# Performance work log

Measured on AMD Instinct MI355X. Metric: run time of the kernel, lower is better.

## Reference

```python
import jax, jax.numpy as jnp
import numpy as np

B, L, D, C, N, K = 4096, 4096, 1024, 64, 8192, 5
TEMP = 0.1
ALPHA = 2.0
EPS = 1e-12


def setup_inputs() -> dict:
    key = jax.random.key(0)
    ks = jax.random.split(key, 8)
    x = jax.random.normal(ks[0], (B, 1, L), jnp.float32)
    y = jax.random.randint(ks[1], (B,), 0, C)
    Wf = jax.random.normal(ks[2], (L, D), jnp.float32) * 0.02
    Wc = jax.random.normal(ks[3], (C, D), jnp.float32) * 0.02
    bc = jnp.zeros((C,), jnp.float32)
    supports_old = jax.random.normal(ks[4], (N, D), jnp.float32)
    scores_old = jax.nn.softmax(jax.random.normal(ks[5], (N, C), jnp.float32), axis=-1)
    labels_old = jax.nn.one_hot(jax.random.randint(ks[6], (N,), 0, C), C, dtype=jnp.float32)
    return dict(x=x, y=y, Wf=Wf, Wc=Wc, bc=bc, supports_old=supports_old,
                labels_old=labels_old, scores_old=scores_old)


def _l2n(v, axis):
    return v / jnp.maximum(jnp.linalg.norm(v, axis=axis, keepdims=True), EPS)


def _masked_mean(v, w):
    return jnp.sum(v * w) / jnp.maximum(jnp.sum(w), 1.0)


def _tta_loss(x, Wf, Wc, bc, supports_old, labels_old, scores_old):
    feats = x.reshape(B, L) @ Wf                      # [B, D] featurizer
    logits = feats @ Wc.T + bc                        # [B, C]
    probs = jax.nn.softmax(logits, -1)
    logp = jax.nn.log_softmax(logits, -1)
    prob = probs.max(-1)
    pred = jnp.argmax(logits, -1)
    # prediction-confidence filter
    y_certain = prob >= prob.mean()
    # input-energy entropy filter (scipy.stats.entropy over axis=2)
    px = x * x
    px = px / jnp.maximum(px.sum(2, keepdims=True), EPS)
    e = -(px * jnp.log(px + 1e-30)).sum(2).reshape(B)
    e_certain = e < e.mean()
    w_c = (e_certain & y_certain).astype(jnp.float32)  # certain mask as weights
    w_u = 1.0 - w_c
    yhat = jax.nn.one_hot(pred, C, dtype=jnp.float32)
    # --- memory bank concat + prototype build (no_grad in torch) ---
    sup_all = jnp.concatenate([supports_old, feats], 0)        # [N+B, D]
    lab_all = jnp.concatenate([labels_old, yhat], 0)           # [N+B, C]
    w_all = jnp.concatenate([jnp.ones((N,), jnp.float32), w_c], 0)
    lw = lab_all * w_all[:, None]
    protos = _l2n(sup_all, 1).T @ lw / jnp.maximum(lw.sum(0, keepdims=True), EPS)
    protos = jax.lax.stop_gradient(_l2n(protos, 0))            # [D, C]
    # --- loss1: Tsallis entropy - diversity on balanced probs ---
    m = jnp.sum(probs * w_c[:, None], 0) / jnp.maximum(w_c.sum(), 1.0)
    pb = probs / jnp.maximum(m, EPS)
    pb = pb / pb.sum(1, keepdims=True)
    tsallis = jnp.mean((1.0 - jnp.sum(pb ** ALPHA, 1)) / (ALPHA - 1.0))
    pm = pb.mean(0)
    div = -jnp.sum(pm * jnp.log(pm + EPS))
    loss1 = tsallis - div
    # --- loss2: PCL, prototype CE on certain samples (temp=1) ---
    lp = jax.nn.log_softmax(_l2n(feats, 1) @ protos, -1)       # [B, C]
    ce = -jnp.take_along_axis(lp, pred[:, None], 1)[:, 0]
    loss2 = _masked_mean(ce, w_c)
    # --- loss3: NCL, kNN soft targets from memory bank, uncertain rows ---
    scores_all = jax.lax.stop_gradient(jnp.concatenate([scores_old, probs], 0))
    sup_det = jax.lax.stop_gradient(sup_all)
    sim = _l2n(feats, 1) @ _l2n(sup_det, 1).T / TEMP           # [B, N+B]
    sim = jnp.where(w_all[None, :] > 0, sim, -jnp.inf)
    _, idx = jax.lax.top_k(sim, K)                             # [B, K]
    tgt = scores_all[idx].mean(1)                              # [B, C]
    ncl = -(tgt * logp).sum(1)
    loss3 = _masked_mean(ncl, w_u)
    return loss1 + loss2 + loss3


def reference(x, y, Wf, Wc, bc, supports_old, labels_old, scores_old):
    return _tta_loss(x, Wf, Wc, bc, supports_old, labels_old, scores_old)
```

## Files before the change

### kernel.cpp

```cpp
#include <hip/hip_runtime.h>
#include <math.h>

#define BBATCH 4096
#define LLEN   4096
#define DDIM   1024
#define CCLS   64
#define NSUP   8192
#define NTOT   12288
#define FEPS   1e-12f
#define KCHUNK 48
#define KCAND  (KCHUNK*5)

#define SC_SUMP  0
#define SC_SUME  1
#define SC_SUMWC 2
#define SC_TSAL  3
#define SC_L2NUM 4
#define SC_L3NUM 5

typedef _Float16 half4_t __attribute__((ext_vector_type(4)));
typedef _Float16 half8_t __attribute__((ext_vector_type(8)));
typedef float    f32x4   __attribute__((ext_vector_type(4)));
typedef float    f32x16  __attribute__((ext_vector_type(16)));

static const size_t OFF_FEATS  = 0;
static const size_t OFF_FEATP1 = OFF_FEATS  + (size_t)BBATCH*DDIM;
static const size_t OFF_WFTH   = OFF_FEATP1 + (size_t)BBATCH*DDIM;
static const size_t OFF_WFTL   = OFF_WFTH   + (size_t)DDIM*LLEN/2;
static const size_t OFF_PROBS  = OFF_WFTL   + (size_t)DDIM*LLEN/2;
static const size_t OFF_LOGP   = OFF_PROBS  + (size_t)BBATCH*CCLS;
static const size_t OFF_FNORM  = OFF_LOGP   + (size_t)BBATCH*CCLS;
static const size_t OFF_SNORM  = OFF_FNORM  + BBATCH;
static const size_t OFF_PMAX   = OFF_SNORM  + NSUP;
static const size_t OFF_EROW   = OFF_PMAX   + BBATCH;
static const size_t OFF_WC     = OFF_EROW   + BBATCH;
static const size_t OFF_PRED   = OFF_WC     + BBATCH;
static const size_t OFF_RB     = OFF_PRED   + BBATCH;
static const size_t OFF_SNM    = OFF_RB     + BBATCH;
static const size_t OFF_PROTOT = OFF_SNM    + NTOT;
static const size_t OFF_CVAL   = OFF_PROTOT + (size_t)CCLS*DDIM;
static const size_t OFF_CIDX   = OFF_CVAL   + (size_t)BBATCH*KCAND;
static const size_t OFF_ZERO   = OFF_CIDX   + (size_t)BBATCH*KCAND;
static const size_t OFF_MACC   = OFF_ZERO;
static const size_t OFF_PMACC  = OFF_MACC   + CCLS;
static const size_t OFF_COLS   = OFF_PMACC  + CCLS;
static const size_t OFF_SCAL   = OFF_COLS   + CCLS;
static const size_t OFF_PROTUN = OFF_SCAL   + 32;
static const size_t OFF_ZEND   = OFF_PROTUN + (size_t)DDIM*CCLS;
static const size_t OFF_SUPH   = OFF_ZEND;
static const size_t OFF_SUPL   = OFF_SUPH   + (size_t)NSUP*DDIM/2;
static const size_t WS_END     = OFF_SUPL   + (size_t)NSUP*DDIM/2;

__device__ __forceinline__ float waveSum(float v){
  #pragma unroll
  for (int o = 32; o > 0; o >>= 1) v += __shfl_xor(v, o);
  return v;
}
__device__ __forceinline__ float waveMax(float v){
  #pragma unroll
  for (int o = 32; o > 0; o >>= 1) v = fmaxf(v, __shfl_xor(v, o));
  return v;
}
__device__ __forceinline__ float blockSum256(float v, float* sh4){
  v = waveSum(v);
  if ((threadIdx.x & 63) == 0) sh4[threadIdx.x >> 6] = v;
  __syncthreads();
  float r = sh4[0] + sh4[1] + sh4[2] + sh4[3];
  __syncthreads();
  return r;
}
__device__ __forceinline__ void top5_insert(float* v, int* ix, float s, int si){
  bool c0 = s > v[0], c1 = s > v[1], c2 = s > v[2], c3 = s > v[3], c4 = s > v[4];
  v[4] = c4 ? (c3 ? v[3] : s) : v[4];  ix[4] = c4 ? (c3 ? ix[3] : si) : ix[4];
  v[3] = c3 ? (c2 ? v[2] : s) : v[3];  ix[3] = c3 ? (c2 ? ix[2] : si) : ix[3];
  v[2] = c2 ? (c1 ? v[1] : s) : v[2];  ix[2] = c2 ? (c1 ? ix[1] : si) : ix[2];
  v[1] = c1 ? (c0 ? v[0] : s) : v[1];  ix[1] = c1 ? (c0 ? ix[0] : si) : ix[1];
  v[0] = c0 ? s : v[0];                ix[0] = c0 ? si : ix[0];
}
__device__ __forceinline__ void split4(const float4 v, half4_t* h, half4_t* l){
  half4_t hh, ll;
  hh[0] = (_Float16)v.x; hh[1] = (_Float16)v.y; hh[2] = (_Float16)v.z; hh[3] = (_Float16)v.w;
  ll[0] = (_Float16)(v.x - (float)hh[0]);
  ll[1] = (_Float16)(v.y - (float)hh[1]);
  ll[2] = (_Float16)(v.z - (float)hh[2]);
  ll[3] = (_Float16)(v.w - (float)hh[3]);
  *h = hh; *l = ll;
}
__device__ __forceinline__ void split8(const float4 a, const float4 b,
                                       half8_t* h, half8_t* l){
  half8_t hh, ll;
  hh[0]=(_Float16)a.x; hh[1]=(_Float16)a.y; hh[2]=(_Float16)a.z; hh[3]=(_Float16)a.w;
  hh[4]=(_Float16)b.x; hh[5]=(_Float16)b.y; hh[6]=(_Float16)b.z; hh[7]=(_Float16)b.w;
  ll[0]=(_Float16)(a.x-(float)hh[0]); ll[1]=(_Float16)(a.y-(float)hh[1]);
  ll[2]=(_Float16)(a.z-(float)hh[2]); ll[3]=(_Float16)(a.w-(float)hh[3]);
  ll[4]=(_Float16)(b.x-(float)hh[4]); ll[5]=(_Float16)(b.y-(float)hh[5]);
  ll[6]=(_Float16)(b.z-(float)hh[6]); ll[7]=(_Float16)(b.w-(float)hh[7]);
  *h = hh; *l = ll;
}

__global__ __launch_bounds__(256)
void k_entropy(const float* __restrict__ x, float* __restrict__ e_row,
               float* __restrict__ scal){
  __shared__ __align__(16) float lx[LLEN];
  __shared__ float sh4[4];
  int row = blockIdx.x, t = threadIdx.x;
  const float4* xr = (const float4*)(x + (size_t)row * LLEN);
  float s = 0.f;
  #pragma unroll
  for (int i = 0; i < 4; ++i){
    float4 v = xr[t + 256*i];
    ((float4*)lx)[t + 256*i] = v;
    s += v.x*v.x + v.y*v.y + v.z*v.z + v.w*v.w;
  }
  s = blockSum256(s, sh4);
  float inv = 1.0f / fmaxf(s, FEPS);
  float ent = 0.f;
  #pragma unroll
  for (int i = 0; i < 4; ++i){
    float4 v = ((float4*)lx)[t + 256*i];
    float p;
    p = v.x*v.x*inv; ent -= p * logf(p + 1e-30f);
    p = v.y*v.y*inv; ent -= p * logf(p + 1e-30f);
    p = v.z*v.z*inv; ent -= p * logf(p + 1e-30f);
    p = v.w*v.w*inv; ent -= p * logf(p + 1e-30f);
  }
  ent = blockSum256(ent, sh4);
  if (t == 0){ e_row[row] = ent; atomicAdd(&scal[SC_SUME], ent); }
}

__global__ __launch_bounds__(256)
void k_wft(const float* __restrict__ Wf, unsigned short* __restrict__ WftH,
           unsigned short* __restrict__ WftL){
  __shared__ __align__(16) float ld[64*68];
  int t = threadIdx.x;
  int d0 = blockIdx.x * 64;
  int l0 = blockIdx.y * 64;
  #pragma unroll
  for (int i = 0; i < 4; ++i){
    int flat = t + 256*i;
    int l = flat >> 4, d4 = (flat & 15) * 4;
    *(float4*)&ld[l*68 + d4] = *(const float4*)(Wf + (size_t)(l0+l)*DDIM + d0 + d4);
  }
  __syncthreads();
  #pragma unroll
  for (int i = 0; i < 4; ++i){
    int flat = t + 256*i;
    int d = flat >> 4, l4 = (flat & 15) * 4;
    float4 v = make_float4(ld[(l4+0)*68 + d], ld[(l4+1)*68 + d],
                           ld[(l4+2)*68 + d], ld[(l4+3)*68 + d]);
    half4_t h, l;
    split4(v, &h, &l);
    *(half4_t*)(WftH + (size_t)(d0+d)*LLEN + l0 + l4) = h;
    *(half4_t*)(WftL + (size_t)(d0+d)*LLEN + l0 + l4) = l;
  }
}

#define SUBH 4096

__global__ __launch_bounds__(256)
void k_feats_mfma(const float* __restrict__ X, const unsigned short* __restrict__ WftHu,
                  const unsigned short* __restrict__ WftLu, float* __restrict__ featp){
  __shared__ __align__(16) _Float16 lds[2*4*SUBH];
  int t = threadIdx.x;
  int n0 = blockIdx.x * 128;
  int m0 = blockIdx.y * 128;
  int kz = blockIdx.z;
  int w = t >> 6, lane = t & 63;
  int wr = w >> 1, wc = w & 1;
  int l31 = lane & 31, hi = lane >> 5;
  const _Float16* Bgh = (const _Float16*)WftHu + (size_t)n0*LLEN;
  const _Float16* Bgl = (const _Float16*)WftLu + (size_t)n0*LLEN;
  const size_t glRow = (size_t)(lane >> 2)*LLEN;
  int ra = t >> 1;
  int kg8 = (t & 1) * 16;
  int aswz = (ra >> 3) & 3;
  const float* Ag = X + (size_t)(m0 + ra)*LLEN + kg8;
  f32x16 acc[2][2];
  #pragma unroll
  for (int i=0;i<2;++i){
    #pragma unroll
    for (int j=0;j<2;++j) acc[i][j] = (f32x16)(0.f);
  }
  const int kstart = kz*2048;

  #define STAGE_B(bufi, k0c) do {                                                 \
    _Float16* Lb = lds + (bufi)*(4*SUBH);                                         \
    _Pragma("unroll")                                                             \
    for (int s2 = 0; s2 < 2; ++s2){                                               \
      int blk = s2*4 + w;                                                         \
      int csrc = (lane & 3) ^ ((blk*2 + (lane >> 5)) & 3);                        \
      size_t go = glRow + (size_t)blk*16*LLEN + (k0c) + (size_t)csrc*8;           \
      __builtin_amdgcn_global_load_lds(                                           \
        (const __attribute__((address_space(1))) void*)(Bgh + go),                \
        (__attribute__((address_space(3))) void*)(Lb + 2*SUBH + blk*512), 16,0,0);\
      __builtin_amdgcn_global_load_lds(                                           \
        (const __attribute__((address_space(1))) void*)(Bgl + go),                \
        (__attribute__((address_space(3))) void*)(Lb + 3*SUBH + blk*512), 16,0,0);\
    }                                                                             \
  } while(0)

  STAGE_B(0, kstart);
  float4 avs[4];
  #pragma unroll
  for (int i=0;i<4;++i) avs[i] = *(const float4*)(Ag + kstart + 4*i);
  int cur = 0;
  int swz = (l31 >> 3) & 3;
  for (int it = 0; it < 64; ++it){
    _Float16* Ah = lds + cur*(4*SUBH);
    _Float16* Al = Ah + SUBH;
    #pragma unroll
    for (int c2 = 0; c2 < 2; ++c2){
      half8_t hv, lv;
      split8(avs[2*c2], avs[2*c2+1], &hv, &lv);
      int slot = ((kg8 >> 3) + c2) ^ aswz;
      *(half8_t*)&Ah[ra*32 + slot*8] = hv;
      *(half8_t*)&Al[ra*32 + slot*8] = lv;
    }
    __syncthreads();
    if (it < 63){
      int kn = kstart + (it+1)*32;
      STAGE_B(cur ^ 1, kn);
      #pragma unroll
      for (int i=0;i<4;++i) avs[i] = *(const float4*)(Ag + kn + 4*i);
      __builtin_amdgcn_sched_barrier(0);
    }
    const _Float16* Bh = lds + cur*(4*SUBH) + 2*SUBH;
    const _Float16* Bl = Bh + SUBH;
    #pragma unroll
    for (int kf = 0; kf < 2; ++kf){
      int sc = (kf*2 + hi) ^ swz;
      half8_t ahf[2], alf[2], bhf[2], blf[2];
      #pragma unroll
      for (int mi=0;mi<2;++mi){
        int off = (wr*64 + mi*32 + l31)*32 + sc*8;
        ahf[mi] = *(const half8_t*)&Ah[off];
        alf[mi] = *(const half8_t*)&Al[off];
      }
      #pragma unroll
      for (int ni=0;ni<2;++ni){
        int off = (wc*64 + ni*32 + l31)*32 + sc*8;
        bhf[ni] = *(const half8_t*)&Bh[off];
        blf[ni] = *(const half8_t*)&Bl[off];
      }
      #pragma unroll
      for (int mi=0;mi<2;++mi){
        #pragma unroll
        for (int ni=0;ni<2;++ni){
          acc[mi][ni] = __builtin_amdgcn_mfma_f32_32x32x16_f16(ahf[mi], bhf[ni], acc[mi][ni], 0,0,0);
          acc[mi][ni] = __builtin_amdgcn_mfma_f32_32x32x16_f16(ahf[mi], blf[ni], acc[mi][ni], 0,0,0);
          acc[mi][ni] = __builtin_amdgcn_mfma_f32_32x32x16_f16(alf[mi], bhf[ni], acc[mi][ni], 0,0,0);
        }
      }
    }
    cur ^= 1;
  }
  #undef STAGE_B
  float* outp = featp + (size_t)kz * BBATCH * DDIM;
  #pragma unroll
  for (int mi=0;mi<2;++mi){
    #pragma unroll
    for (int ni=0;ni<2;++ni){
      #pragma unroll
      for (int r=0;r<16;++r){
        int row = m0 + wr*64 + mi*32 + (r&3) + 8*(r>>2) + 4*hi;
        int col = n0 + wc*64 + ni*32 + l31;
        outp[(size_t)row*DDIM + col] = acc[mi][ni][r];
      }
    }
  }
}

__global__ __launch_bounds__(256)
void k_supnorm(const float* __restrict__ sup, float* __restrict__ snorm,
               _Float16* __restrict__ suph, _Float16* __restrict__ supl){
  int w = threadIdx.x >> 6, lane = threadIdx.x & 63;
  int row = blockIdx.x*4 + w;
  const float4* rp = (const float4*)(sup + (size_t)row * DDIM);
  float s = 0.f;
  #pragma unroll
  for (int j=0;j<4;++j){
    float4 v = rp[lane + 64*j];
    half4_t h, l;
    split4(v, &h, &l);
    *(half4_t*)(suph + (size_t)row*DDIM + (lane + 64*j)*4) = h;
    *(half4_t*)(supl + (size_t)row*DDIM + (lane + 64*j)*4) = l;
    s += v.x*v.x+v.y*v.y+v.z*v.z+v.w*v.w;
  }
  s = waveSum(s);
  if (lane==0) snorm[row] = sqrtf(s);
}

__global__ __launch_bounds__(256)
void k_logits(float* __restrict__ feats, const float* __restrict__ featp1,
              const float* __restrict__ Wc,
              const float* __restrict__ bc, float* __restrict__ probs,
              float* __restrict__ logp, float* __restrict__ pmax,
              int* __restrict__ pred, float* __restrict__ fnorm,
              float* __restrict__ scal,
              _Float16* __restrict__ fh, _Float16* __restrict__ fl){
  __shared__ __align__(16) float f[DDIM];
  __shared__ float z[CCLS];
  __shared__ float sh4[4];
  int row = blockIdx.x, t = threadIdx.x;
  const float4* fr0 = (const float4*)(feats  + (size_t)row * DDIM);
  const float4* fr1 = (const float4*)(featp1 + (size_t)row * DDIM);
  float ss = 0.f;
  { float4 a = fr0[t], b = fr1[t];
    float4 v = make_float4(a.x+b.x, a.y+b.y, a.z+b.z, a.w+b.w);
    ((float4*)f)[t] = v;
    ((float4*)(feats + (size_t)row*DDIM))[t] = v;
    half4_t h, l;
    split4(v, &h, &l);
    *(half4_t*)(fh + (size_t)row*DDIM + t*4) = h;
    *(half4_t*)(fl + (size_t)row*DDIM + t*4) = l;
    ss += v.x*v.x+v.y*v.y+v.z*v.z+v.w*v.w; }
  ss = blockSum256(ss, sh4);
  if (t==0) fnorm[row] = sqrtf(ss);
  int w = t >> 6, lane = t & 63;
  for (int ci = 0; ci < 16; ++ci){
    int c = w*16 + ci;
    const float4* wc = (const float4*)(Wc + (size_t)c * DDIM);
    float d = 0.f;
    #pragma unroll
    for (int j=0;j<4;++j){
      float4 a = wc[lane + 64*j];
      float4 b = ((float4*)f)[lane + 64*j];
      d += a.x*b.x+a.y*b.y+a.z*b.z+a.w*b.w;
    }
    d = waveSum(d);
    if (lane == 0) z[c] = d + bc[c];
  }
  __syncthreads();
  if (w == 0){
    float zz = z[lane];
    float m = waveMax(zz);
    unsigned long long bal = __ballot(zz == m);
    int am = __ffsll(bal) - 1;
    float ex = expf(zz - m);
    float sv = waveSum(ex);
    probs[(size_t)row*CCLS + lane] = ex / sv;
    logp[(size_t)row*CCLS + lane]  = (zz - m) - logf(sv);
    if (lane == 0){
      float pmv = 1.0f / sv;
      pmax[row] = pmv;
      pred[row] = am;
      atomicAdd(&scal[SC_SUMP], pmv);
    }
  }
}

__global__ __launch_bounds__(256)
void k_mask(const float* __restrict__ e_row, const float* __restrict__ pmax,
            const float* __restrict__ fnorm, const float* __restrict__ snorm,
            const int* __restrict__ pred, float* __restrict__ w_c,
            float* __restrict__ rb, float* __restrict__ snm,
            float* __restrict__ colsum, float* __restrict__ scal){
  int i = blockIdx.x * 256 + threadIdx.x;
  if (i < NSUP) snm[i] = 1.0f / fmaxf(snorm[i], FEPS);
  if (i < BBATCH){
    float me = scal[SC_SUME] * (1.0f/BBATCH);
    float mp = scal[SC_SUMP] * (1.0f/BBATCH);
    float wc = ((e_row[i] < me) && (pmax[i] >= mp)) ? 1.0f : 0.0f;
    w_c[i] = wc;
    float fn = fmaxf(fnorm[i], FEPS);
    rb[i] = 10.0f / fn;
    snm[NSUP + i] = (wc > 0.f) ? (1.0f / fn) : -1.0f;
    atomicAdd(&scal[SC_SUMWC], wc);
    atomicAdd(&colsum[pred[i]], wc);
  }
}

__global__ __launch_bounds__(256)
void k_colsum_labels(const float* __restrict__ labels, float* __restrict__ colsum){
  int t = threadIdx.x, c = t & 63, sub = t >> 6;
  int r0 = blockIdx.x * 256;
  float s = 0.f;
  for (int i = 0; i < 64; ++i){
    int r = r0 + sub + 4*i;
    s += labels[(size_t)r*CCLS + c];
  }
  __shared__ float loc[4][64];
  loc[sub][c] = s;
  __syncthreads();
  if (sub == 0) atomicAdd(&colsum[c], loc[0][c]+loc[1][c]+loc[2][c]+loc[3][c]);
}

__global__ __launch_bounds__(256)
void k_m_accum(const float* __restrict__ probs, const float* __restrict__ w_c,
               float* __restrict__ m_acc){
  int t = threadIdx.x, c = t & 63, sub = t >> 6;
  int r0 = blockIdx.x * 64;
  float s = 0.f;
  for (int i = 0; i < 16; ++i){
    int r = r0 + sub + 4*i;
    s += probs[(size_t)r*CCLS + c] * w_c[r];
  }
  __shared__ float loc[4][64];
  loc[sub][c] = s;
  __syncthreads();
  if (sub == 0) atomicAdd(&m_acc[c], loc[0][c]+loc[1][c]+loc[2][c]+loc[3][c]);
}

__global__ __launch_bounds__(256)
void k_loss1(const float* __restrict__ probs, const float* __restrict__ m_acc,
             float* __restrict__ pm_acc, float* __restrict__ scal){
  int t = threadIdx.x, w = t >> 6, lane = t & 63;
  float swc = fmaxf(scal[SC_SUMWC], 1.0f);
  float minv = 1.0f / fmaxf(m_acc[lane] / swc, FEPS);
  float pml = 0.f, tsl = 0.f;
  int r0 = blockIdx.x * 64 + w * 16;
  for (int i = 0; i < 16; ++i){
    int r = r0 + i;
    float pb = probs[(size_t)r*CCLS + lane] * minv;
    float t1 = waveSum(pb);
    float t2 = waveSum(pb*pb);
    tsl += 1.0f - t2/(t1*t1);
    pml += pb/t1;
  }
  atomicAdd(&pm_acc[lane], pml);
  if (lane == 0) atomicAdd(&scal[SC_TSAL], tsl);
}

__global__ __launch_bounds__(256)
void k_protos_gemm(const float* __restrict__ sup, const float* __restrict__ feats,
                   const float* __restrict__ labels, const int* __restrict__ pred,
                   const float* __restrict__ w_c, const float* __restrict__ snm,
                   float* __restrict__ protos_un){
  __shared__ __align__(16) float ssx[64*68];
  __shared__ __align__(16) float sl[64*68];
  int t = threadIdx.x;
  int d0 = blockIdx.x * 64;
  int nbase = blockIdx.y * 1536;
  int dg = t & 15, cg = t >> 4;
  float acc[4][4];
  #pragma unroll
  for (int i=0;i<4;++i){
    #pragma unroll
    for (int j=0;j<4;++j) acc[i][j]=0.f;
  }
  for (int n0 = 0; n0 < 1536; n0 += 64){
    __syncthreads();
    #pragma unroll
    for (int i = 0; i < 4; ++i){
      int fidx = t + 256*i;
      int r = fidx >> 4;
      int dc = (fidx & 15) * 4;
      int n = nbase + n0 + r;
      const float* rp = (n < NSUP) ? (sup + (size_t)n*DDIM)
                                   : (feats + (size_t)(n-NSUP)*DDIM);
      *(float4*)&ssx[r*68 + dc] = *(const float4*)(rp + d0 + dc);
    }
    #pragma unroll
    for (int i = 0; i < 4; ++i){
      int fidx = t + 256*i;
      int r = fidx >> 4;
      int cc = (fidx & 15) * 4;
      int n = nbase + n0 + r;
      float sc = snm[n];
      float4 v;
      if (n < NSUP){
        float4 lb = *(const float4*)(labels + (size_t)n*CCLS + cc);
        v.x = lb.x*sc; v.y = lb.y*sc; v.z = lb.z*sc; v.w = lb.w*sc;
      } else {
        int b = n - NSUP;
        float base = w_c[b] * sc;
        int p = pred[b];
        v.x = (p == cc+0) ? base : 0.f;
        v.y = (p == cc+1) ? base : 0.f;
        v.z = (p == cc+2) ? base : 0.f;
        v.w = (p == cc+3) ? base : 0.f;
      }
      *(float4*)&sl[r*68 + cc] = v;
    }
    __syncthreads();
    #pragma unroll 4
    for (int kk = 0; kk < 64; ++kk){
      float4 a = *(float4*)&ssx[kk*68 + 4*dg];
      float4 b = *(float4*)&sl[kk*68 + 4*cg];
      float av[4] = {a.x,a.y,a.z,a.w};
      float bv[4] = {b.x,b.y,b.z,b.w};
      #pragma unroll
      for (int i=0;i<4;++i){
        #pragma unroll
        for (int j=0;j<4;++j) acc[i][j] = fmaf(av[i], bv[j], acc[i][j]);
      }
    }
  }
  #pragma unroll
  for (int i=0;i<4;++i){
    #pragma unroll
    for (int j=0;j<4;++j)
      atomicAdd(&protos_un[(size_t)(d0 + 4*dg + i)*CCLS + 4*cg + j], acc[i][j]);
  }
}

__global__ __launch_bounds__(256)
void k_protos_norm(const float* __restrict__ protos_un, const float* __restrict__ colsum,
                   float* __restrict__ protos_t){
  int c = blockIdx.x, t = threadIdx.x;
  __shared__ float sh4[4];
  float cs = fmaxf(colsum[c], FEPS);
  float v[4];
  float ss = 0.f;
  #pragma unroll
  for (int i=0;i<4;++i){
    int d = t + 256*i;
    v[i] = protos_un[(size_t)d*CCLS + c] / cs;
    ss += v[i]*v[i];
  }
  ss = blockSum256(ss, sh4);
  float inv = 1.0f / fmaxf(sqrtf(ss), FEPS);
  #pragma unroll
  for (int i=0;i<4;++i){
    int d = t + 256*i;
    protos_t[(size_t)c*DDIM + d] = v[i]*inv;
  }
}

__global__ __launch_bounds__(256)
void k_loss2(const float* __restrict__ feats, const float* __restrict__ protos_t,
             const int* __restrict__ pred, const float* __restrict__ w_c,
             const float* __restrict__ fnorm, float* __restrict__ scal){
  int row = blockIdx.x, t = threadIdx.x;
  float wc = w_c[row];
  if (wc == 0.f) return;
  __shared__ __align__(16) float f[DDIM];
  __shared__ float z[CCLS];
  float inv = 1.0f / fmaxf(fnorm[row], FEPS);
  { float4 v = ((const float4*)(feats + (size_t)row*DDIM))[t];
    v.x*=inv; v.y*=inv; v.z*=inv; v.w*=inv;
    ((float4*)f)[t] = v; }
  __syncthreads();
  int w = t >> 6, lane = t & 63;
  for (int ci=0; ci<16; ++ci){
    int c = w*16+ci;
    const float4* pc = (const float4*)(protos_t + (size_t)c*DDIM);
    float d = 0.f;
    #pragma unroll
    for (int j=0;j<4;++j){
      float4 a = pc[lane + 64*j];
      float4 b = ((float4*)f)[lane + 64*j];
      d += a.x*b.x+a.y*b.y+a.z*b.z+a.w*b.w;
    }
    d = waveSum(d);
    if (lane==0) z[c] = d;
  }
  __syncthreads();
  if (w == 0){
    float zz = z[lane];
    float m = waveMax(zz);
    float sv = waveSum(expf(zz - m));
    if (lane == 0){
      float lse = m + logf(sv);
      float ce = lse - z[pred[row]];
      atomicAdd(&scal[SC_L2NUM], ce * wc);
    }
  }
}

#define SIMTILES 32
__global__ __launch_bounds__(512, 2)
void k_sim_mfma(const _Float16* __restrict__ fh, const _Float16* __restrict__ fl,
                const _Float16* __restrict__ suph, const _Float16* __restrict__ supl,
                const float* __restrict__ rb, const float* __restrict__ snm,
                float* __restrict__ cval, int* __restrict__ cidx){
  __shared__ __align__(16) _Float16 lds[2*32768];
  __shared__ float sns[256];
  int t = threadIdx.x;
  int w = t >> 6, lane = t & 63;
  int wr = w >> 2, wcn = w & 3;
  int l31 = lane & 31, hi = lane >> 5;
  int bidl = blockIdx.y * 48 + blockIdx.x;
  int xcd = bidl & 7, lin = bidl >> 3;
  int yb = xcd * 2 + (lin / 48);
  int xb = lin - (lin / 48) * 48;
  int m0 = xb * 256, n0 = yb * 256;
  if (t < 256) sns[t] = snm[m0 + t];
  const _Float16 *Agh, *Agl;
  if (xb < 32){ Agh = suph + (size_t)m0*DDIM; Agl = supl + (size_t)m0*DDIM; }
  else        { Agh = fh + (size_t)(m0-NSUP)*DDIM; Agl = fl + (size_t)(m0-NSUP)*DDIM; }
  const _Float16* Bgh = fh + (size_t)n0*DDIM;
  const _Float16* Bgl = fl + (size_t)n0*DDIM;
  int Rlo = w*16 + (lane>>2), Rhi = 128 + Rlo;
  size_t offLo = (size_t)Rlo*DDIM + (size_t)((((lane&3) ^ ((Rlo>>3)&3))) * 8);
  size_t offHi = (size_t)Rhi*DDIM + (size_t)((((lane&3) ^ ((Rhi>>3)&3))) * 8);
  const _Float16* srcArr[4] = {Agh, Agl, Bgh, Bgl};
  f32x16 acc[4][2];
  #pragma unroll
  for (int i=0;i<4;++i){
    #pragma unroll
    for (int j=0;j<2;++j) acc[i][j] = (f32x16)(0.f);
  }

  #define SIM_STAGE(b, c, kt) do {                                                \
    const _Float16* sp = srcArr[(c)>>1] + (((c)&1) ? offHi : offLo)               \
                         + (size_t)(kt)*32;                                       \
    __builtin_amdgcn_global_load_lds(                                             \
      (const __attribute__((address_space(1))) void*)sp,                          \
      (__attribute__((address_space(3))) void*)(lds + (b)*32768 + ((c)>>1)*8192   \
                                                + ((c)&1)*4096 + w*512), 16,0,0); \
  } while(0)

  SIM_STAGE(0,0,0); SIM_STAGE(0,1,0); SIM_STAGE(0,2,0); SIM_STAGE(0,3,0);
  SIM_STAGE(0,4,0); SIM_STAGE(0,5,0); SIM_STAGE(0,6,0); SIM_STAGE(0,7,0);

  for (int kt = 0; kt < SIMTILES; ++kt){
    const _Float16* buf = lds + (kt&1)*32768;
    int nb = (kt+1)&1;
    asm volatile("s_waitcnt vmcnt(0)" ::: "memory");
    __builtin_amdgcn_s_barrier();
    __builtin_amdgcn_sched_barrier(0);
    half8_t bh[2][2], bl[2][2];
    #pragma unroll
    for (int ni=0;ni<2;++ni){
      int Rb = wcn*64 + ni*32 + l31;
      int swB = (Rb>>3)&3;
      const _Float16* pbh = buf + 16384 + Rb*32;
      const _Float16* pbl = buf + 24576 + Rb*32;
      #pragma unroll
      for (int k=0;k<2;++k){
        int s = ((k*2+hi)^swB)*8;
        bh[ni][k] = *(const half8_t*)(pbh + s);
        bl[ni][k] = *(const half8_t*)(pbl + s);
      }
    }
    #pragma unroll
    for (int p=0;p<4;++p){
      int Ra = wr*128 + p*32 + l31;
      int swA = (Ra>>3)&3;
      const _Float16* pah = buf + Ra*32;
      const _Float16* pal = buf + 8192 + Ra*32;
      half8_t ah[2], al[2];
      #pragma unroll
      for (int k=0;k<2;++k){
        int s = ((k*2+hi)^swA)*8;
        ah[k] = *(const half8_t*)(pah + s);
        al[k] = *(const half8_t*)(pal + s);
      }
      if (kt < SIMTILES-1){
        if (p==0){ SIM_STAGE(nb,0,kt+1); SIM_STAGE(nb,1,kt+1); }
        else if (p==1){ SIM_STAGE(nb,2,kt+1); SIM_STAGE(nb,3,kt+1); SIM_STAGE(nb,4,kt+1); }
        else if (p==2){ SIM_STAGE(nb,5,kt+1); SIM_STAGE(nb,6,kt+1); SIM_STAGE(nb,7,kt+1); }
      }
      __builtin_amdgcn_s_setprio(1);
      #pragma unroll
      for (int k=0;k<2;++k){
        #pragma unroll
        for (int ni=0;ni<2;++ni){
          acc[p][ni] = __builtin_amdgcn_mfma_f32_32x32x16_f16(ah[k], bh[ni][k], acc[p][ni], 0,0,0);
          acc[p][ni] = __builtin_amdgcn_mfma_f32_32x32x16_f16(ah[k], bl[ni][k], acc[p][ni], 0,0,0);
          acc[p][ni] = __builtin_amdgcn_mfma_f32_32x32x16_f16(al[k], bh[ni][k], acc[p][ni], 0,0,0);
        }
      }
      __builtin_amdgcn_s_setprio(0);
      __builtin_amdgcn_sched_barrier(0);
    }
  }
  #undef SIM_STAGE
  __syncthreads();
  float tv[2][5]; int ti[2][5];
  #pragma unroll
  for (int ni=0;ni<2;++ni){
    #pragma unroll
    for (int k=0;k<5;++k){ tv[ni][k] = -INFINITY; ti[ni][k] = 0x7fffffff; }
  }
  #pragma unroll
  for (int ni=0;ni<2;++ni){
    float rbv = rb[n0 + wcn*64 + ni*32 + l31];
    #pragma unroll
    for (int mi=0;mi<4;++mi){
      #pragma unroll
      for (int r=0;r<16;++r){
        int rl = wr*128 + mi*32 + (r&3) + 8*(r>>2) + 4*hi;
        float sn = sns[rl];
        float v = acc[mi][ni][r] * rbv * fabsf(sn);
        v = (sn > 0.f) ? v : -INFINITY;
        top5_insert(tv[ni], ti[ni], v, m0 + rl);
      }
    }
  }
  #pragma unroll
  for (int ni=0;ni<2;++ni){
    float pv[5]; int pi[5];
    #pragma unroll
    for (int k=0;k<5;++k){ pv[k] = __shfl_xor(tv[ni][k], 32); pi[k] = __shfl_xor(ti[ni][k], 32); }
    #pragma unroll
    for (int k=0;k<5;++k) top5_insert(tv[ni], ti[ni], pv[k], pi[k]);
  }
  float* MV = (float*)lds;
  int*   MI = (int*)(lds + 5120);
  if (hi == 0){
    #pragma unroll
    for (int ni=0;ni<2;++ni){
      int col = wcn*64 + ni*32 + l31;
      #pragma unroll
      for (int k=0;k<5;++k){
        MV[(col*2 + wr)*5 + k] = tv[ni][k];
        MI[(col*2 + wr)*5 + k] = ti[ni][k];
      }
    }
  }
  __syncthreads();
  if (t < 256){
    float bv[5]; int bi[5];
    #pragma unroll
    for (int k=0;k<5;++k){ bv[k] = MV[(t*2+0)*5 + k]; bi[k] = MI[(t*2+0)*5 + k]; }
    #pragma unroll
    for (int k=0;k<5;++k) top5_insert(bv, bi, MV[(t*2+1)*5 + k], MI[(t*2+1)*5 + k]);
    float* co = cval + (size_t)(n0 + t)*KCAND + xb*5;
    int*   ci = cidx + (size_t)(n0 + t)*KCAND + xb*5;
    #pragma unroll
    for (int k=0;k<5;++k){ co[k] = bv[k]; ci[k] = bi[k]; }
  }
}

__global__ __launch_bounds__(256)
void k_merge_ncl(const float* __restrict__ cval, const int* __restrict__ cidx,
                 const float* __restrict__ scores_old, const float* __restrict__ probs,
                 const float* __restrict__ logp, const float* __restrict__ w_c,
                 float* __restrict__ scal){
  int t = threadIdx.x, w = t >> 6, lane = t & 63;
  int b = blockIdx.x*4 + w;
  float bv[5]; int bi[5];
  #pragma unroll
  for (int k=0;k<5;++k){ bv[k] = -INFINITY; bi[k] = 0x7fffffff; }
  #pragma unroll
  for (int it = 0; it < 4; ++it){
    int j = lane + 64*it;
    if (j < KCAND)
      top5_insert(bv, bi, cval[(size_t)b*KCAND + j], cidx[(size_t)b*KCAND + j]);
  }
  #pragma unroll
  for (int off = 32; off > 0; off >>= 1){
    float pv[5]; int pi[5];
    #pragma unroll
    for (int k=0;k<5;++k){ pv[k] = __shfl_xor(bv[k], off); pi[k] = __shfl_xor(bi[k], off); }
    #pragma unroll
    for (int k=0;k<5;++k) top5_insert(bv, bi, pv[k], pi[k]);
  }
  float tg = 0.f;
  #pragma unroll
  for (int k=0;k<5;++k){
    int ix = bi[k];
    const float* srow = (ix < NSUP) ? (scores_old + (size_t)ix*CCLS)
                                    : (probs + (size_t)(ix-NSUP)*CCLS);
    tg += srow[lane];
  }
  tg *= 0.2f;
  float d = tg * logp[(size_t)b*CCLS + lane];
  d = waveSum(d);
  if (lane == 0) atomicAdd(&scal[SC_L3NUM], -d * (1.0f - w_c[b]));
}

__global__ void k_final(const float* __restrict__ pm_acc, const float* __restrict__ scal,
                        float* __restrict__ out){
  int lane = threadIdx.x;
  float pm = pm_acc[lane] * (1.0f/BBATCH);
  float dterm = pm * logf(pm + FEPS);
  float dv = waveSum(dterm);
  if (lane == 0){
    float div = -dv;
    float tsallis = scal[SC_TSAL] * (1.0f/BBATCH);
    float swc = scal[SC_SUMWC];
    float l1 = tsallis - div;
    float l2 = scal[SC_L2NUM] / fmaxf(swc, 1.0f);
    float l3 = scal[SC_L3NUM] / fmaxf((float)BBATCH - swc, 1.0f);
    out[0] = l1 + l2 + l3;
  }
}

extern "C" void kernel_launch(void* const* d_in, const int* in_sizes, int n_in,
                              void* d_out, int out_size, void* d_ws, size_t ws_size,
                              hipStream_t stream){
  (void)in_sizes; (void)n_in; (void)out_size; (void)ws_size;
  const float* x      = (const float*)d_in[0];
  const float* Wf     = (const float*)d_in[2];
  const float* Wc     = (const float*)d_in[3];
  const float* bc     = (const float*)d_in[4];
  const float* sup    = (const float*)d_in[5];
  const float* labels = (const float*)d_in[6];
  const float* scores = (const float*)d_in[7];
  float* ws = (float*)d_ws;

  float* feats  = ws + OFF_FEATS;
  float* featp1 = ws + OFF_FEATP1;
  unsigned short* wfth = (unsigned short*)(ws + OFF_WFTH);
  unsigned short* wftl = (unsigned short*)(ws + OFF_WFTL);
  _Float16* feat_h = (_Float16*)(ws + OFF_WFTH);
  _Float16* feat_l = (_Float16*)(ws + OFF_WFTL);
  _Float16* sup_h  = (_Float16*)(ws + OFF_SUPH);
  _Float16* sup_l  = (_Float16*)(ws + OFF_SUPL);
  float* probs  = ws + OFF_PROBS;
  float* logp   = ws + OFF_LOGP;
  float* fnorm  = ws + OFF_FNORM;
  float* snorm  = ws + OFF_SNORM;
  float* pmax   = ws + OFF_PMAX;
  float* e_row  = ws + OFF_EROW;
  float* w_c    = ws + OFF_WC;
  int*   pred   = (int*)(ws + OFF_PRED);
  float* rb     = ws + OFF_RB;
  float* snm    = ws + OFF_SNM;
  float* protot = ws + OFF_PROTOT;
  float* cvalp  = ws + OFF_CVAL;
  int*   cidxp  = (int*)(ws + OFF_CIDX);
  float* m_acc  = ws + OFF_MACC;
  float* pm_acc = ws + OFF_PMACC;
  float* colsum = ws + OFF_COLS;
  float* scal   = ws + OFF_SCAL;
  float* protun = ws + OFF_PROTUN;

  hipMemsetAsync(ws + OFF_ZERO, 0, (OFF_ZEND - OFF_ZERO)*sizeof(float), stream);

  k_entropy      <<<BBATCH, 256, 0, stream>>>(x, e_row, scal);
  k_wft          <<<dim3(DDIM/64, LLEN/64), 256, 0, stream>>>(Wf, wfth, wftl);
  k_feats_mfma   <<<dim3(DDIM/128, BBATCH/128, 2), 256, 0, stream>>>(x, wfth, wftl, feats);
  k_supnorm      <<<NSUP/4, 256, 0, stream>>>(sup, snorm, sup_h, sup_l);
  k_logits       <<<BBATCH, 256, 0, stream>>>(feats, featp1, Wc, bc, probs, logp, pmax, pred, fnorm, scal, feat_h, feat_l);
  k_mask         <<<32, 256, 0, stream>>>(e_row, pmax, fnorm, snorm, pred, w_c, rb, snm, colsum, scal);
  k_colsum_labels<<<32, 256, 0, stream>>>(labels, colsum);
  k_m_accum      <<<64, 256, 0, stream>>>(probs, w_c, m_acc);
  k_loss1        <<<64, 256, 0, stream>>>(probs, m_acc, pm_acc, scal);
  k_protos_gemm  <<<dim3(16, 8), 256, 0, stream>>>(sup, feats, labels, pred, w_c, snm, protun);
  k_protos_norm  <<<CCLS, 256, 0, stream>>>(protun, colsum, protot);
  k_loss2        <<<BBATCH, 256, 0, stream>>>(feats, protot, pred, w_c, fnorm, scal);
  k_sim_mfma     <<<dim3(48, 16), 512, 0, stream>>>(feat_h, feat_l, sup_h, sup_l, rb, snm, cvalp, cidxp);
  k_merge_ncl    <<<BBATCH/4, 256, 0, stream>>>(cvalp, cidxp, scores, probs, logp, w_c, scal);
  k_final        <<<1, 64, 0, stream>>>(pm_acc, scal, (float*)d_out);
}
```

Baseline: 921.9 us.

## Use single-fp16 similarity GEMM for top-6 candidates, rescore top-10 in fp32

The similarity GEMM previously used a split hi/lo fp16 scheme with three MFMAs per product to emulate fp32. It now uses only the hi fp16 halves, one MFMA, 1024-thread blocks and a smaller LDS footprint. To make up for the lower precision it keeps 6 candidates per chunk instead of 5, takes the approximate top-10 per row, recomputes those dot products exactly in fp32 and then picks the final top-5. This cuts MFMA work and global traffic for the GEMM by about a factor of three, at the cost of a gather-heavy rescore pass and a small risk of picking the wrong neighbours if a true top-5 element falls outside the approximate top-10.

```diff
diff --git a/kernel.cpp b/kernel.cpp
--- a/kernel.cpp
+++ b/kernel.cpp
@@ -9,7 +9,7 @@
 #define NTOT   12288
 #define FEPS   1e-12f
 #define KCHUNK 48
-#define KCAND  (KCHUNK*5)
+#define KCAND  (KCHUNK*6)
 
 #define SC_SUMP  0
 #define SC_SUME  1
@@ -69,13 +69,14 @@
   __syncthreads();
   return r;
 }
-__device__ __forceinline__ void top5_insert(float* v, int* ix, float s, int si){
-  bool c0 = s > v[0], c1 = s > v[1], c2 = s > v[2], c3 = s > v[3], c4 = s > v[4];
-  v[4] = c4 ? (c3 ? v[3] : s) : v[4];  ix[4] = c4 ? (c3 ? ix[3] : si) : ix[4];
-  v[3] = c3 ? (c2 ? v[2] : s) : v[3];  ix[3] = c3 ? (c2 ? ix[2] : si) : ix[3];
-  v[2] = c2 ? (c1 ? v[1] : s) : v[2];  ix[2] = c2 ? (c1 ? ix[1] : si) : ix[2];
-  v[1] = c1 ? (c0 ? v[0] : s) : v[1];  ix[1] = c1 ? (c0 ? ix[0] : si) : ix[1];
-  v[0] = c0 ? s : v[0];                ix[0] = c0 ? si : ix[0];
+__device__ __forceinline__ void top6_insert(float* v, int* ix, float s, int si){
+  bool c0=s>v[0],c1=s>v[1],c2=s>v[2],c3=s>v[3],c4=s>v[4],c5=s>v[5];
+  v[5]=c5?(c4?v[4]:s):v[5]; ix[5]=c5?(c4?ix[4]:si):ix[5];
+  v[4]=c4?(c3?v[3]:s):v[4]; ix[4]=c4?(c3?ix[3]:si):ix[4];
+  v[3]=c3?(c2?v[2]:s):v[3]; ix[3]=c3?(c2?ix[2]:si):ix[3];
+  v[2]=c2?(c1?v[1]:s):v[2]; ix[2]=c2?(c1?ix[1]:si):ix[2];
+  v[1]=c1?(c0?v[0]:s):v[1]; ix[1]=c1?(c0?ix[0]:si):ix[1];
+  v[0]=c0?s:v[0];           ix[0]=c0?si:ix[0];
 }
 __device__ __forceinline__ void split4(const float4 v, half4_t* h, half4_t* l){
   half4_t hh, ll;
@@ -558,13 +559,11 @@
   }
 }
 
-#define SIMTILES 32
-__global__ __launch_bounds__(512, 2)
-void k_sim_mfma(const _Float16* __restrict__ fh, const _Float16* __restrict__ fl,
-                const _Float16* __restrict__ suph, const _Float16* __restrict__ supl,
-                const float* __restrict__ rb, const float* __restrict__ snm,
-                float* __restrict__ cval, int* __restrict__ cidx){
-  __shared__ __align__(16) _Float16 lds[2*32768];
+__global__ __launch_bounds__(1024, 1)
+void k_sim_approx(const _Float16* __restrict__ fh, const _Float16* __restrict__ suph,
+                  const float* __restrict__ snm,
+                  float* __restrict__ cval, int* __restrict__ cidx){
+  __shared__ __align__(16) _Float16 lds[2*16384];
   __shared__ float sns[256];
   int t = threadIdx.x;
   int w = t >> 6, lane = t & 63;
@@ -576,172 +575,208 @@
   int xb = lin - (lin / 48) * 48;
   int m0 = xb * 256, n0 = yb * 256;
   if (t < 256) sns[t] = snm[m0 + t];
-  const _Float16 *Agh, *Agl;
-  if (xb < 32){ Agh = suph + (size_t)m0*DDIM; Agl = supl + (size_t)m0*DDIM; }
-  else        { Agh = fh + (size_t)(m0-NSUP)*DDIM; Agl = fl + (size_t)(m0-NSUP)*DDIM; }
-  const _Float16* Bgh = fh + (size_t)n0*DDIM;
-  const _Float16* Bgl = fl + (size_t)n0*DDIM;
-  int Rlo = w*16 + (lane>>2), Rhi = 128 + Rlo;
-  size_t offLo = (size_t)Rlo*DDIM + (size_t)((((lane&3) ^ ((Rlo>>3)&3))) * 8);
-  size_t offHi = (size_t)Rhi*DDIM + (size_t)((((lane&3) ^ ((Rhi>>3)&3))) * 8);
-  const _Float16* srcArr[4] = {Agh, Agl, Bgh, Bgl};
-  f32x16 acc[4][2];
-  #pragma unroll
-  for (int i=0;i<4;++i){
+  const _Float16* Ag = (xb < 32) ? (suph + (size_t)m0*DDIM)
+                                 : (fh + (size_t)(m0-NSUP)*DDIM);
+  const _Float16* Bg = fh + (size_t)n0*DDIM;
+  int Rs = w*16 + (lane>>2);
+  int cs = (lane & 3) ^ ((Rs >> 3) & 3);
+  const size_t offS = (size_t)Rs*DDIM + (size_t)cs*8;
+  f32x16 acc[2][2];
+  #pragma unroll
+  for (int i=0;i<2;++i){
     #pragma unroll
     for (int j=0;j<2;++j) acc[i][j] = (f32x16)(0.f);
   }
 
-  #define SIM_STAGE(b, c, kt) do {                                                \
-    const _Float16* sp = srcArr[(c)>>1] + (((c)&1) ? offHi : offLo)               \
-                         + (size_t)(kt)*32;                                       \
+  #define SIM_ST(b, kt) do {                                                      \
     __builtin_amdgcn_global_load_lds(                                             \
-      (const __attribute__((address_space(1))) void*)sp,                          \
-      (__attribute__((address_space(3))) void*)(lds + (b)*32768 + ((c)>>1)*8192   \
-                                                + ((c)&1)*4096 + w*512), 16,0,0); \
+      (const __attribute__((address_space(1))) void*)(Ag + offS + (size_t)(kt)*32),\
+      (__attribute__((address_space(3))) void*)(lds + (b)*16384 + w*512), 16,0,0);\
+    __builtin_amdgcn_global_load_lds(                                             \
+      (const __attribute__((address_space(1))) void*)(Bg + offS + (size_t)(kt)*32),\
+      (__attribute__((address_space(3))) void*)(lds + (b)*16384 + 8192 + w*512), 16,0,0);\
   } while(0)
 
-  SIM_STAGE(0,0,0); SIM_STAGE(0,1,0); SIM_STAGE(0,2,0); SIM_STAGE(0,3,0);
-  SIM_STAGE(0,4,0); SIM_STAGE(0,5,0); SIM_STAGE(0,6,0); SIM_STAGE(0,7,0);
-
-  for (int kt = 0; kt < SIMTILES; ++kt){
-    const _Float16* buf = lds + (kt&1)*32768;
-    int nb = (kt+1)&1;
-    asm volatile("s_waitcnt vmcnt(0)" ::: "memory");
-    __builtin_amdgcn_s_barrier();
-    __builtin_amdgcn_sched_barrier(0);
-    half8_t bh[2][2], bl[2][2];
+  SIM_ST(0, 0);
+  for (int kt = 0; kt < 32; ++kt){
+    const _Float16* buf = lds + (kt&1)*16384;
+    __syncthreads();
+    half8_t af[2][2], bf[2][2];
+    #pragma unroll
+    for (int p=0;p<2;++p){
+      int Ra = wr*64 + p*32 + l31;
+      int sw = (Ra>>3)&3;
+      #pragma unroll
+      for (int kf=0;kf<2;++kf)
+        af[p][kf] = *(const half8_t*)(buf + Ra*32 + (((kf*2+hi)^sw))*8);
+    }
     #pragma unroll
     for (int ni=0;ni<2;++ni){
       int Rb = wcn*64 + ni*32 + l31;
-      int swB = (Rb>>3)&3;
-      const _Float16* pbh = buf + 16384 + Rb*32;
-      const _Float16* pbl = buf + 24576 + Rb*32;
-      #pragma unroll
-      for (int k=0;k<2;++k){
-        int s = ((k*2+hi)^swB)*8;
-        bh[ni][k] = *(const half8_t*)(pbh + s);
-        bl[ni][k] = *(const half8_t*)(pbl + s);
+      int sw = (Rb>>3)&3;
+      #pragma unroll
+      for (int kf=0;kf<2;++kf)
+        bf[ni][kf] = *(const half8_t*)(buf + 8192 + Rb*32 + (((kf*2+hi)^sw))*8);
+    }
+    if (kt < 31) SIM_ST((kt+1)&1, kt+1);
+    __builtin_amdgcn_s_setprio(1);
+    #pragma unroll
+    for (int p=0;p<2;++p){
+      #pragma unroll
+      for (int ni=0;ni<2;++ni){
+        #pragma unroll
+        for (int kf=0;kf<2;++kf)
+          acc[p][ni] = __builtin_amdgcn_mfma_f32_32x32x16_f16(af[p][kf], bf[ni][kf], acc[p][ni], 0,0,0);
       }
     }
-    #pragma unroll
-    for (int p=0;p<4;++p){
-      int Ra = wr*128 + p*32 + l31;
-      int swA = (Ra>>3)&3;
-      const _Float16* pah = buf + Ra*32;
-      const _Float16* pal = buf + 8192 + Ra*32;
-      half8_t ah[2], al[2];
-      #pragma unroll
-      for (int k=0;k<2;++k){
-        int s = ((k*2+hi)^swA)*8;
-        ah[k] = *(const half8_t*)(pah + s);
-        al[k] = *(const half8_t*)(pal + s);
+    __builtin_amdgcn_s_setprio(0);
+  }
+  #undef SIM_ST
+  __syncthreads();
+  float tv[2][6]; int ti[2][6];
+  #pragma unroll
+  for (int ni=0;ni<2;++ni){
+    #pragma unroll
+    for (int k=0;k<6;++k){ tv[ni][k] = -INFINITY; ti[ni][k] = 0x7fffffff; }
+  }
+  #pragma unroll
+  for (int ni=0;ni<2;++ni){
+    #pragma unroll
+    for (int p=0;p<2;++p){
+      #pragma unroll
+      for (int r=0;r<16;++r){
+        int rl = wr*64 + p*32 + (r&3) + 8*(r>>2) + 4*hi;
+        float sn = sns[rl];
+        float v = acc[p][ni][r] * fabsf(sn);
+        v = (sn > 0.f) ? v : -INFINITY;
+        top6_insert(tv[ni], ti[ni], v, m0 + rl);
       }
-      if (kt < SIMTILES-1){
-        if (p==0){ SIM_STAGE(nb,0,kt+1); SIM_STAGE(nb,1,kt+1); }
-        else if (p==1){ SIM_STAGE(nb,2,kt+1); SIM_STAGE(nb,3,kt+1); SIM_STAGE(nb,4,kt+1); }
-        else if (p==2){ SIM_STAGE(nb,5,kt+1); SIM_STAGE(nb,6,kt+1); SIM_STAGE(nb,7,kt+1); }
-      }
-      __builtin_amdgcn_s_setprio(1);
-      #pragma unroll
-      for (int k=0;k<2;++k){
-        #pragma unroll
-        for (int ni=0;ni<2;++ni){
-          acc[p][ni] = __builtin_amdgcn_mfma_f32_32x32x16_f16(ah[k], bh[ni][k], acc[p][ni], 0,0,0);
-          acc[p][ni] = __builtin_amdgcn_mfma_f32_32x32x16_f16(ah[k], bl[ni][k], acc[p][ni], 0,0,0);
-          acc[p][ni] = __builtin_amdgcn_mfma_f32_32x32x16_f16(al[k], bh[ni][k], acc[p][ni], 0,0,0);
-        }
-      }
-      __builtin_amdgcn_s_setprio(0);
-      __builtin_amdgcn_sched_barrier(0);
-    }
-  }
-  #undef SIM_STAGE
-  __syncthreads();
-  float tv[2][5]; int ti[2][5];
+    }
+  }
   #pragma unroll
   for (int ni=0;ni<2;++ni){
-    #pragma unroll
-    for (int k=0;k<5;++k){ tv[ni][k] = -INFINITY; ti[ni][k] = 0x7fffffff; }
-  }
-  #pragma unroll
-  for (int ni=0;ni<2;++ni){
-    float rbv = rb[n0 + wcn*64 + ni*32 + l31];
-    #pragma unroll
-    for (int mi=0;mi<4;++mi){
-      #pragma unroll
-      for (int r=0;r<16;++r){
-        int rl = wr*128 + mi*32 + (r&3) + 8*(r>>2) + 4*hi;
-        float sn = sns[rl];
-        float v = acc[mi][ni][r] * rbv * fabsf(sn);
-        v = (sn > 0.f) ? v : -INFINITY;
-        top5_insert(tv[ni], ti[ni], v, m0 + rl);
-      }
-    }
-  }
-  #pragma unroll
-  for (int ni=0;ni<2;++ni){
-    float pv[5]; int pi[5];
-    #pragma unroll
-    for (int k=0;k<5;++k){ pv[k] = __shfl_xor(tv[ni][k], 32); pi[k] = __shfl_xor(ti[ni][k], 32); }
-    #pragma unroll
-    for (int k=0;k<5;++k) top5_insert(tv[ni], ti[ni], pv[k], pi[k]);
+    float pv[6]; int pi[6];
+    #pragma unroll
+    for (int k=0;k<6;++k){ pv[k] = __shfl_xor(tv[ni][k], 32); pi[k] = __shfl_xor(ti[ni][k], 32); }
+    #pragma unroll
+    for (int k=0;k<6;++k) top6_insert(tv[ni], ti[ni], pv[k], pi[k]);
   }
   float* MV = (float*)lds;
-  int*   MI = (int*)(lds + 5120);
+  int*   MI = (int*)((char*)lds + 24576);
   if (hi == 0){
     #pragma unroll
     for (int ni=0;ni<2;++ni){
       int col = wcn*64 + ni*32 + l31;
       #pragma unroll
-      for (int k=0;k<5;++k){
-        MV[(col*2 + wr)*5 + k] = tv[ni][k];
-        MI[(col*2 + wr)*5 + k] = ti[ni][k];
+      for (int k=0;k<6;++k){
+        MV[(col*4 + wr)*6 + k] = tv[ni][k];
+        MI[(col*4 + wr)*6 + k] = ti[ni][k];
       }
     }
   }
   __syncthreads();
   if (t < 256){
-    float bv[5]; int bi[5];
-    #pragma unroll
-    for (int k=0;k<5;++k){ bv[k] = MV[(t*2+0)*5 + k]; bi[k] = MI[(t*2+0)*5 + k]; }
-    #pragma unroll
-    for (int k=0;k<5;++k) top5_insert(bv, bi, MV[(t*2+1)*5 + k], MI[(t*2+1)*5 + k]);
-    float* co = cval + (size_t)(n0 + t)*KCAND + xb*5;
-    int*   ci = cidx + (size_t)(n0 + t)*KCAND + xb*5;
-    #pragma unroll
-    for (int k=0;k<5;++k){ co[k] = bv[k]; ci[k] = bi[k]; }
-  }
-}
-
-__global__ __launch_bounds__(256)
-void k_merge_ncl(const float* __restrict__ cval, const int* __restrict__ cidx,
-                 const float* __restrict__ scores_old, const float* __restrict__ probs,
-                 const float* __restrict__ logp, const float* __restrict__ w_c,
-                 float* __restrict__ scal){
+    float bv[6]; int bi[6];
+    #pragma unroll
+    for (int k=0;k<6;++k){ bv[k] = -INFINITY; bi[k] = 0x7fffffff; }
+    for (int j = 0; j < 24; ++j) top6_insert(bv, bi, MV[t*24 + j], MI[t*24 + j]);
+    float* co = cval + (size_t)(n0 + t)*KCAND + xb*6;
+    int*   ci = cidx + (size_t)(n0 + t)*KCAND + xb*6;
+    #pragma unroll
+    for (int k=0;k<6;++k){ co[k] = bv[k]; ci[k] = bi[k]; }
+  }
+}
+
+__global__ __launch_bounds__(256)
+void k_rescore_ncl(const float* __restrict__ cval, const int* __restrict__ cidx,
+                   const float* __restrict__ sup, const float* __restrict__ feats,
+                   const float* __restrict__ rb, const float* __restrict__ snm,
+                   const float* __restrict__ scores_old, const float* __restrict__ probs,
+                   const float* __restrict__ logp, const float* __restrict__ w_c,
+                   float* __restrict__ scal){
   int t = threadIdx.x, w = t >> 6, lane = t & 63;
   int b = blockIdx.x*4 + w;
-  float bv[5]; int bi[5];
-  #pragma unroll
-  for (int k=0;k<5;++k){ bv[k] = -INFINITY; bi[k] = 0x7fffffff; }
-  #pragma unroll
-  for (int it = 0; it < 4; ++it){
-    int j = lane + 64*it;
-    if (j < KCAND)
-      top5_insert(bv, bi, cval[(size_t)b*KCAND + j], cidx[(size_t)b*KCAND + j]);
-  }
-  #pragma unroll
-  for (int off = 32; off > 0; off >>= 1){
-    float pv[5]; int pi[5];
-    #pragma unroll
-    for (int k=0;k<5;++k){ pv[k] = __shfl_xor(bv[k], off); pi[k] = __shfl_xor(bi[k], off); }
-    #pragma unroll
-    for (int k=0;k<5;++k) top5_insert(bv, bi, pv[k], pi[k]);
+  float lv[5]; int li[5];
+  #pragma unroll
+  for (int j=0;j<5;++j){
+    int idx = lane + 64*j;
+    bool ok = idx < KCAND;
+    lv[j] = ok ? cval[(size_t)b*KCAND + idx] : -INFINITY;
+    li[j] = ok ? cidx[(size_t)b*KCAND + idx] : 0x7fffffff;
+  }
+  #pragma unroll
+  for (int a=0;a<4;++a){
+    #pragma unroll
+    for (int c=0;c<4-a;++c){
+      bool sw = lv[c+1] > lv[c];
+      float fv = sw ? lv[c+1] : lv[c];  float fw = sw ? lv[c] : lv[c+1];
+      int   iv = sw ? li[c+1] : li[c];  int   iw = sw ? li[c] : li[c+1];
+      lv[c]=fv; lv[c+1]=fw; li[c]=iv; li[c+1]=iw;
+    }
+  }
+  float t10v[10]; int t10i[10];
+  int head = 0;
+  #pragma unroll
+  for (int k=0;k<10;++k){
+    float hv = -INFINITY; int hidx = 0x7fffffff;
+    switch(head){
+      case 0: hv=lv[0]; hidx=li[0]; break;
+      case 1: hv=lv[1]; hidx=li[1]; break;
+      case 2: hv=lv[2]; hidx=li[2]; break;
+      case 3: hv=lv[3]; hidx=li[3]; break;
+      case 4: hv=lv[4]; hidx=li[4]; break;
+      default: break;
+    }
+    float m = waveMax(hv);
+    unsigned long long bal = __ballot(hv == m);
+    int wl = __ffsll(bal) - 1;
+    t10v[k] = m;
+    t10i[k] = __shfl(hidx, wl);
+    if (lane == wl) head++;
+  }
+  (void)t10v;
+  float4 fr0 = *(const float4*)(feats + (size_t)b*DDIM + lane*16);
+  float4 fr1 = *(const float4*)(feats + (size_t)b*DDIM + lane*16 + 4);
+  float4 fr2 = *(const float4*)(feats + (size_t)b*DDIM + lane*16 + 8);
+  float4 fr3 = *(const float4*)(feats + (size_t)b*DDIM + lane*16 + 12);
+  float rbv = rb[b];
+  float ev[10];
+  #pragma unroll
+  for (int c=0;c<10;++c){
+    int idx = t10i[c];
+    const float* srow = (idx < NSUP) ? (sup + (size_t)idx*DDIM)
+                                     : (feats + (size_t)(idx-NSUP)*DDIM);
+    float4 s0 = *(const float4*)(srow + lane*16);
+    float4 s1 = *(const float4*)(srow + lane*16 + 4);
+    float4 s2 = *(const float4*)(srow + lane*16 + 8);
+    float4 s3 = *(const float4*)(srow + lane*16 + 12);
+    float d = fr0.x*s0.x + fr0.y*s0.y + fr0.z*s0.z + fr0.w*s0.w
+            + fr1.x*s1.x + fr1.y*s1.y + fr1.z*s1.z + fr1.w*s1.w
+            + fr2.x*s2.x + fr2.y*s2.y + fr2.z*s2.z + fr2.w*s2.w
+            + fr3.x*s3.x + fr3.y*s3.y + fr3.z*s3.z + fr3.w*s3.w;
+    d = waveSum(d);
+    ev[c] = d * rbv * fabsf(snm[idx]);
+  }
+  int used = 0;
+  int sel[5];
+  #pragma unroll
+  for (int k=0;k<5;++k){
+    float bb = -INFINITY; int bbi = 0x7fffffff; int bj = 0;
+    #pragma unroll
+    for (int j=0;j<10;++j){
+      bool free_ = !((used >> j) & 1);
+      bool better = free_ && ((ev[j] > bb) || (ev[j] == bb && t10i[j] < bbi));
+      bb  = better ? ev[j]   : bb;
+      bbi = better ? t10i[j] : bbi;
+      bj  = better ? j       : bj;
+    }
+    used |= (1 << bj);
+    sel[k] = bbi;
   }
   float tg = 0.f;
   #pragma unroll
   for (int k=0;k<5;++k){
-    int ix = bi[k];
+    int ix = sel[k];
     const float* srow = (ix < NSUP) ? (scores_old + (size_t)ix*CCLS)
                                     : (probs + (size_t)(ix-NSUP)*CCLS);
     tg += srow[lane];
@@ -823,7 +858,7 @@
   k_protos_gemm  <<<dim3(16, 8), 256, 0, stream>>>(sup, feats, labels, pred, w_c, snm, protun);
   k_protos_norm  <<<CCLS, 256, 0, stream>>>(protun, colsum, protot);
   k_loss2        <<<BBATCH, 256, 0, stream>>>(feats, protot, pred, w_c, fnorm, scal);
-  k_sim_mfma     <<<dim3(48, 16), 512, 0, stream>>>(feat_h, feat_l, sup_h, sup_l, rb, snm, cvalp, cidxp);
-  k_merge_ncl    <<<BBATCH/4, 256, 0, stream>>>(cvalp, cidxp, scores, probs, logp, w_c, scal);
+  k_sim_approx   <<<dim3(48, 16), 1024, 0, stream>>>(feat_h, sup_h, snm, cvalp, cidxp);
+  k_rescore_ncl  <<<BBATCH/4, 256, 0, stream>>>(cvalp, cidxp, sup, feats, rb, snm, scores, probs, logp, w_c, scal);
   k_final        <<<1, 64, 0, stream>>>(pm_acc, scal, (float*)d_out);
 }
```

Measured after the change: 826.7 us. -10.3%, faster.
